# Performance work log

Measured on AMD Instinct MI355X. Metric: run time of the kernel, lower is better.

The kernel has to match this reference:

```python
import jax, jax.numpy as jnp
import numpy as np

EPS = 1e-6
QMAX = 127.0  # hif8 emulated as symmetric 8-bit fake-quant (true hif8 numerics are proprietary)


def _rotate_half(v):
    d = v.shape[-1] // 2
    return jnp.concatenate([-v[..., d:], v[..., :d]], axis=-1)


def _quant(v):
    # per-row (last-axis) absmax quantization emulating hif8 with a per-tensor-row scale
    amax = jnp.max(jnp.abs(v), axis=-1, keepdims=True)
    scale = jnp.maximum(amax / QMAX, 1e-8)
    q = jnp.round(v / scale)
    return q, jnp.squeeze(scale, -1)


def setup_inputs() -> dict:
    key = jax.random.key(0)
    ks = jax.random.split(key, 16)
    B, S, H, Hn, D, L = 2, 4096, 2048, 32, 128, 16384
    return {
        "x": jax.random.normal(ks[0], (B, S, H), jnp.float32),
        "q_norm": jax.random.uniform(ks[1], (H,), jnp.float32),
        "q_norm_scale": jax.random.uniform(ks[2], (H,), jnp.float32),
        "w_qb": jax.random.normal(ks[3], (H, Hn * D), jnp.float32),
        "w_qb_scale": jax.random.uniform(ks[4], (Hn * D,), jnp.float32),
        "wk": jax.random.normal(ks[5], (H, D), jnp.float32),
        "w_proj": jax.random.normal(ks[6], (H, Hn), jnp.float32),
        "ln_gamma_k": jax.random.uniform(ks[7], (H,), jnp.float32),
        "ln_beta_k": jax.random.normal(ks[8], (H,), jnp.float32),
        "cos_idx_rope": jax.random.uniform(ks[9], (S, D), jnp.float32),
        "sin_idx_rope": jax.random.uniform(ks[10], (S, D), jnp.float32),
        "hadamard_q": jax.random.normal(ks[11], (D, D), jnp.float32),
        "hadamard_k": jax.random.normal(ks[12], (D, D), jnp.float32),
        "k_cache": jnp.zeros((L, D), jnp.float32),
        "k_cache_scale": jnp.zeros((L,), jnp.float32),
        "k_cache_index": jnp.arange(B * S, dtype=jnp.int32).reshape(B, S),
    }


def reference(x, q_norm, q_norm_scale, w_qb, w_qb_scale, wk, w_proj,
              ln_gamma_k, ln_beta_k, cos_idx_rope, sin_idx_rope,
              hadamard_q, hadamard_k, k_cache, k_cache_scale, k_cache_index):
    B, S, H = x.shape
    D = hadamard_q.shape[0]
    Hn = w_qb.shape[1] // D

    # ---- Q branch: RMSNorm + smooth scale -> quantized GEMM (dequant fused) ----
    rms = jax.lax.rsqrt(jnp.mean(x * x, axis=-1, keepdims=True) + EPS)
    xq = x * rms * q_norm * q_norm_scale                      # [B,S,H]
    q = jnp.einsum('bsh,hd->bsd', xq, w_qb) * w_qb_scale      # [B,S,Hn*D]
    q = q.reshape(B, S, Hn, D)

    cos_q = cos_idx_rope[:S][None, :, None, :]
    sin_q = sin_idx_rope[:S][None, :, None, :]
    q = q * cos_q + _rotate_half(q) * sin_q                   # RoPE
    q = jnp.einsum('bshd,de->bshe', q, hadamard_q)            # Hadamard mix
    q_hif8, q_scale = _quant(q)                               # [B,S,Hn,D], [B,S,Hn]

    # ---- K branch: LayerNorm -> proj -> RoPE -> Hadamard -> quant ----
    mu = jnp.mean(x, axis=-1, keepdims=True)
    var = jnp.mean(jnp.square(x - mu), axis=-1, keepdims=True)
    xk = (x - mu) * jax.lax.rsqrt(var + EPS) * ln_gamma_k + ln_beta_k
    k = jnp.einsum('bsh,hd->bsd', xk, wk)                     # [B,S,D]
    cos_k = cos_idx_rope[:S][None, :, :]
    sin_k = sin_idx_rope[:S][None, :, :]
    k = k * cos_k + _rotate_half(k) * sin_k
    k = jnp.einsum('bsd,de->bse', k, hadamard_k)
    k_q, k_s = _quant(k)                                      # [B,S,D], [B,S]

    # ---- scatter quantized K into the indexer cache ----
    idx = k_cache_index.reshape(-1)
    k_hif8 = k_cache.at[idx].set(k_q.reshape(-1, D))
    k_scale = k_cache_scale.at[idx].set(k_s.reshape(-1))

    # ---- per-head indexer weights ----
    weights = jnp.einsum('bsh,he->bse', x, w_proj)            # [B,S,Hn]

    return (q_hif8, q_scale, k_hif8, k_scale, weights)
```

## Files before the change

### kernel.cpp

```cpp
#include <hip/hip_runtime.h>
#include <hip/hip_bf16.h>
#include <stdint.h>

constexpr int Mrows = 8192;
constexpr int Hdim  = 2048;
constexpr int Sdim  = 4096;
constexpr int HnD   = 4096;
constexpr int Hn    = 32;
constexpr int Dd    = 128;
constexpr int Lc    = 16384;
constexpr int NFULL = 4352;

typedef unsigned short u16;
typedef __attribute__((ext_vector_type(8))) short    bf16x8;
typedef __attribute__((ext_vector_type(4))) float    f32x4;
typedef __attribute__((ext_vector_type(8))) unsigned short u16x8;

__device__ __forceinline__ float bf2f(u16 u) {
    union { unsigned int i; float f; } v; v.i = ((unsigned int)u) << 16; return v.f;
}
__device__ __forceinline__ u16 f2bf(float f) {
    union { float f; unsigned int i; } v; v.f = f;
    unsigned int x = v.i;
    return (u16)((x + 0x7fffu + ((x >> 16) & 1u)) >> 16);
}
__device__ __forceinline__ void gload_lds16(const void* g, void* l) {
    __builtin_amdgcn_global_load_lds(
        (const __attribute__((address_space(1))) void*)g,
        (__attribute__((address_space(3))) void*)l, 16, 0, 0);
}

__global__ __launch_bounds__(256) void stats_cvt(
    const float* __restrict__ x, u16* __restrict__ xb, float* __restrict__ rms,
    float* __restrict__ mu, float* __restrict__ rstd)
{
    int r = blockIdx.x, t = threadIdx.x;
    const float4* xr = (const float4*)(x + (size_t)r * Hdim);
    float4 a = xr[2 * t], bq = xr[2 * t + 1];
    float v[8] = {a.x, a.y, a.z, a.w, bq.x, bq.y, bq.z, bq.w};
    float s = 0.f, ss = 0.f;
    __align__(16) u16 o[8];
    #pragma unroll
    for (int i = 0; i < 8; i++) { s += v[i]; ss += v[i] * v[i]; o[i] = f2bf(v[i]); }
    ((u16x8*)(xb + (size_t)r * Hdim))[t] = *(const u16x8*)o;
    for (int oo = 32; oo > 0; oo >>= 1) { s += __shfl_down(s, oo); ss += __shfl_down(ss, oo); }
    __shared__ float as[4], ass[4];
    if ((t & 63) == 0) { as[t >> 6] = s; ass[t >> 6] = ss; }
    __syncthreads();
    if (t == 0) {
        float S1 = as[0] + as[1] + as[2] + as[3];
        float S2 = ass[0] + ass[1] + ass[2] + ass[3];
        float mean = S1 / Hdim, msq = S2 / Hdim;
        rms[r]  = rsqrtf(msq + 1e-6f);
        mu[r]   = mean;
        rstd[r] = rsqrtf(msq - mean * mean + 1e-6f);
    }
}

__global__ __launch_bounds__(256) void prep_wt(
    const float* __restrict__ wqb, const float* __restrict__ qn, const float* __restrict__ qns,
    const float* __restrict__ wk,  const float* __restrict__ g,  const float* __restrict__ wproj,
    u16* __restrict__ wt)
{
    __shared__ u16 tile[64][72];
    int k0 = blockIdx.x * 64, n0 = blockIdx.y * 64;
    int t = threadIdx.x;
    int lk = t >> 2, lc0 = (t & 3) * 16;
    int k = k0 + lk;
    float c1k = qn[k] * qns[k];
    float gk  = g[k];
    #pragma unroll
    for (int i = 0; i < 16; i++) {
        int n = n0 + lc0 + i;
        float val;
        if (n < 4096)      val = wqb[(size_t)k * HnD + n] * c1k;
        else if (n < 4224) val = wk[k * Dd + (n - 4096)] * gk;
        else if (n < 4256) val = wproj[k * Hn + (n - 4224)];
        else               val = 0.f;
        tile[lk][lc0 + i] = f2bf(val);
    }
    __syncthreads();
    int ln = t >> 2, lk0 = (t & 3) * 16;
    __align__(16) u16 o[16];
    #pragma unroll
    for (int i = 0; i < 16; i++) o[i] = tile[lk0 + i][ln];
    u16* dst = wt + (size_t)(n0 + ln) * Hdim + k0 + lk0;
    *(u16x8*)dst = *(const u16x8*)o;
    *(u16x8*)(dst + 8) = *((const u16x8*)o + 1);
}

__global__ __launch_bounds__(256) void transpose_h(
    const float* __restrict__ hq, const float* __restrict__ hk,
    u16* __restrict__ hqt, u16* __restrict__ hkt)
{
    __shared__ float tile[128][129];
    const float* src = blockIdx.x ? hk : hq;
    u16* dst = blockIdx.x ? hkt : hqt;
    int t = threadIdx.x;
    int r = t >> 1, h = (t & 1) * 64;
    #pragma unroll
    for (int j = 0; j < 16; j++) {
        float4 v = *(const float4*)(src + r * Dd + h + 4 * j);
        tile[r][h + 4 * j]     = v.x;
        tile[r][h + 4 * j + 1] = v.y;
        tile[r][h + 4 * j + 2] = v.z;
        tile[r][h + 4 * j + 3] = v.w;
    }
    __syncthreads();
    #pragma unroll
    for (int j0 = 0; j0 < 64; j0 += 8) {
        __align__(16) u16 o[8];
        #pragma unroll
        for (int j = 0; j < 8; j++) o[j] = f2bf(tile[h + j0 + j][r]);
        *(u16x8*)(dst + r * Dd + h + j0) = *(const u16x8*)o;
    }
}

__global__ __launch_bounds__(256) void bg_dot(
    const float* __restrict__ wk, const float* __restrict__ g, const float* __restrict__ b,
    float* __restrict__ bdot, float* __restrict__ gdot)
{
    int n = blockIdx.x, t = threadIdx.x;
    float sb = 0.f, sg = 0.f;
    for (int k = t; k < Hdim; k += 256) {
        float w = wk[k * Dd + n];
        sb += b[k] * w;
        sg += g[k] * w;
    }
    for (int o = 32; o > 0; o >>= 1) { sb += __shfl_down(sb, o); sg += __shfl_down(sg, o); }
    __shared__ float rb[4], rg[4];
    if ((t & 63) == 0) { rb[t >> 6] = sb; rg[t >> 6] = sg; }
    __syncthreads();
    if (t == 0) { bdot[n] = rb[0] + rb[1] + rb[2] + rb[3]; gdot[n] = rg[0] + rg[1] + rg[2] + rg[3]; }
}

#define QLDA(slotb, mt) (*(const bf16x8*)(lds + (slotb) + \
    (wr*64 + (mt)*16 + l15) * 64 + qsw))
#define QLDB(slotb, nt) (*(const bf16x8*)(lds + (slotb) + 8192 + \
    (wc*128 + (nt)*16 + l15) * 64 + qsw))
#define QSTG(slotb, sidx) do { \
    gload_lds16(Ab + (size_t)(arow)       * Hdim + (sidx) * 32 + acol, lds + (slotb) + wq); \
    gload_lds16(Ab + (size_t)(64 + arow)  * Hdim + (sidx) * 32 + acol, lds + (slotb) + 4096 + wq); \
    gload_lds16(Bb + (size_t)(arow)       * Hdim + (sidx) * 32 + acol, lds + (slotb) + 8192 + wq); \
    gload_lds16(Bb + (size_t)(64 + arow)  * Hdim + (sidx) * 32 + acol, lds + (slotb) + 12288 + wq); \
    gload_lds16(Bb + (size_t)(128 + arow) * Hdim + (sidx) * 32 + acol, lds + (slotb) + 16384 + wq); \
    gload_lds16(Bb + (size_t)(192 + arow) * Hdim + (sidx) * 32 + acol, lds + (slotb) + 20480 + wq); \
} while (0)

__global__ __launch_bounds__(256, 2) void main_gemm(
    const u16* __restrict__ A, const u16* __restrict__ Bt,
    const float* __restrict__ rms, const float* __restrict__ qbs,
    const u16* __restrict__ hqt,
    const float* __restrict__ cosr, const float* __restrict__ sinr,
    float* __restrict__ oq, float* __restrict__ oqs)
{
    __shared__ __align__(16) char lds[73728];

    int tid = threadIdx.x;
    int w = tid >> 6, lane = tid & 63, quad = lane >> 4, l15 = lane & 15;
    int wr = w >> 1, wc = w & 1;
    int bm = blockIdx.x, bn = blockIdx.y;
    int brow = bm * 128;
    int qsw = (quad ^ ((l15 >> 1) & 3)) * 16;

    const u16* Ab = A  + (size_t)brow * Hdim;
    const u16* Bb = Bt + (size_t)(bn * 256) * Hdim;

    int arow = tid >> 2;
    int acol = (((tid & 3) ^ ((tid >> 3) & 3)) * 8);
    int wq   = w * 1024;

    f32x4 acc[4][8] = {};

    QSTG(0, 0);
    QSTG(24576, 1);
    asm volatile("s_waitcnt vmcnt(6)" ::: "memory");
    __builtin_amdgcn_sched_barrier(0);
    __builtin_amdgcn_s_barrier();

    int slotb = 0;
    for (int s = 0; s < 64; s++) {
        bf16x8 af[4], bq[8];
        #pragma unroll
        for (int mt = 0; mt < 4; mt++) af[mt] = QLDA(slotb, mt);
        #pragma unroll
        for (int nt = 0; nt < 8; nt++) bq[nt] = QLDB(slotb, nt);
        if (s + 2 < 64) {
            int ns = slotb + 49152; if (ns >= 73728) ns -= 73728;
            QSTG(ns, s + 2);
        }
        asm volatile("s_waitcnt lgkmcnt(0)" ::: "memory");
        __builtin_amdgcn_sched_barrier(0);
        __builtin_amdgcn_s_setprio(1);
        #pragma unroll
        for (int mt = 0; mt < 4; mt++)
            #pragma unroll
            for (int nt = 0; nt < 8; nt++)
                acc[mt][nt] = __builtin_amdgcn_mfma_f32_16x16x32_bf16(af[mt], bq[nt], acc[mt][nt], 0, 0, 0);
        __builtin_amdgcn_s_setprio(0);
        if (s < 62) { asm volatile("s_waitcnt vmcnt(6)" ::: "memory"); }
        else        { asm volatile("s_waitcnt vmcnt(0)" ::: "memory"); }
        __builtin_amdgcn_sched_barrier(0);
        __builtin_amdgcn_s_barrier();
        slotb += 24576; if (slotb >= 73728) slotb -= 73728;
    }

    __syncthreads();
    int head = bn * 2 + wc;
    char* Pw = lds + w * 16384;
    float qb[8];
    #pragma unroll
    for (int nt = 0; nt < 8; nt++) qb[nt] = qbs[head * 128 + nt * 16 + l15];
    #pragma unroll
    for (int mt = 0; mt < 4; mt++) {
        float y[8][4];
        #pragma unroll
        for (int reg = 0; reg < 4; reg++) {
            float rv = rms[brow + wr * 64 + mt * 16 + quad * 4 + reg];
            #pragma unroll
            for (int nt = 0; nt < 8; nt++) y[nt][reg] = acc[mt][nt][reg] * rv * qb[nt];
        }
        #pragma unroll
        for (int reg = 0; reg < 4; reg++) {
            int rp = mt * 16 + quad * 4 + reg;
            int s_ = (brow + wr * 64 + rp) & (Sdim - 1);
            const float* cr = cosr + (size_t)s_ * Dd + l15;
            const float* sr = sinr + (size_t)s_ * Dd + l15;
            int sw = (rp & 7) << 4;
            #pragma unroll
            for (int nt = 0; nt < 8; nt++) {
                float c  = cr[nt * 16];
                float sv = sr[nt * 16];
                float sign = (nt < 4) ? -1.f : 1.f;
                float o = y[nt][reg] * c + sign * y[nt ^ 4][reg] * sv;
                int colb = (nt * 16 + l15) * 2;
                *(u16*)(Pw + rp * 256 + (colb ^ sw)) = f2bf(o);
            }
        }
    }
    __syncthreads();
    #pragma unroll
    for (int mt = 0; mt < 4; mt++) {
        bf16x8 pa[4];
        #pragma unroll
        for (int kb = 0; kb < 4; kb++) {
            int row = mt * 16 + l15;
            pa[kb] = *(const bf16x8*)(Pw + row * 256 + ((kb * 64 + quad * 16) ^ ((row & 7) << 4)));
        }
        f32x4 a2[8] = {};
        #pragma unroll
        for (int nt = 0; nt < 8; nt++) {
            #pragma unroll
            for (int kb = 0; kb < 4; kb++) {
                bf16x8 hb = *(const bf16x8*)(hqt + (size_t)(nt * 16 + l15) * Dd + kb * 32 + quad * 8);
                a2[nt] = __builtin_amdgcn_mfma_f32_16x16x32_bf16(pa[kb], hb, a2[nt], 0, 0, 0);
            }
        }
        #pragma unroll
        for (int reg = 0; reg < 4; reg++) {
            float m = 0.f;
            #pragma unroll
            for (int nt = 0; nt < 8; nt++) m = fmaxf(m, fabsf(a2[nt][reg]));
            m = fmaxf(m, __shfl_xor(m, 8));
            m = fmaxf(m, __shfl_xor(m, 4));
            m = fmaxf(m, __shfl_xor(m, 2));
            m = fmaxf(m, __shfl_xor(m, 1));
            float scale = fmaxf(m * (1.f / 127.f), 1e-8f);
            float inv = 1.f / scale;
            int r = brow + wr * 64 + mt * 16 + quad * 4 + reg;
            float* orow = oq + (size_t)r * HnD + head * 128;
            #pragma unroll
            for (int nt = 0; nt < 8; nt++)
                orow[nt * 16 + l15] = rintf(a2[nt][reg] * inv);
            if (l15 == 0) oqs[(size_t)r * Hn + head] = scale;
        }
    }
}

__global__ __launch_bounds__(256) void kw_gemm(
    const u16* __restrict__ A, const u16* __restrict__ Bt,
    const float* __restrict__ rstd, const float* __restrict__ mu,
    const float* __restrict__ bdot, const float* __restrict__ gdot,
    float* __restrict__ kpre, float* __restrict__ wout)
{
    __shared__ __align__(16) u16 sA[32 * 64];
    __shared__ __align__(16) u16 sB[192 * 64];
    int tid = threadIdx.x, w = tid >> 6, lane = tid & 63, quad = lane >> 4, l15 = lane & 15;
    int blk = blockIdx.x;
    const u16* Ab = A  + (size_t)(blk * 32) * Hdim;
    const u16* Bb = Bt + (size_t)4096 * Hdim;

    f32x4 acc[2][3] = {};

    for (int s = 0; s < 32; s++) {
        __syncthreads();
        {
            int row = tid >> 3, ch = (tid & 7) ^ (row & 7);
            gload_lds16(Ab + (size_t)row * Hdim + s * 64 + ch * 8, (char*)sA + w * 1024);
        }
        #pragma unroll
        for (int u = 0; u < 6; u++) {
            int idx = u * 256 + tid;
            int row = idx >> 3, ch = (idx & 7) ^ (row & 7);
            gload_lds16(Bb + (size_t)row * Hdim + s * 64 + ch * 8,
                        (char*)sB + u * 4096 + w * 1024);
        }
        __syncthreads();
        #pragma unroll
        for (int kk = 0; kk < 2; kk++) {
            bf16x8 af[2], bf[3];
            #pragma unroll
            for (int m = 0; m < 2; m++) {
                int row = m * 16 + l15;
                af[m] = *(const bf16x8*)(sA + row * 64 + (((kk * 4 + quad) ^ (row & 7)) * 8));
            }
            #pragma unroll
            for (int j = 0; j < 3; j++) {
                int row = (w * 3 + j) * 16 + l15;
                bf[j] = *(const bf16x8*)(sB + row * 64 + (((kk * 4 + quad) ^ (row & 7)) * 8));
            }
            #pragma unroll
            for (int m = 0; m < 2; m++)
                #pragma unroll
                for (int j = 0; j < 3; j++)
                    acc[m][j] = __builtin_amdgcn_mfma_f32_16x16x32_bf16(af[m], bf[j], acc[m][j], 0, 0, 0);
        }
    }
    #pragma unroll
    for (int m = 0; m < 2; m++)
        #pragma unroll
        for (int reg = 0; reg < 4; reg++) {
            int r = blk * 32 + m * 16 + quad * 4 + reg;
            float sd = rstd[r], m_ = mu[r];
            #pragma unroll
            for (int j = 0; j < 3; j++) {
                int f = w * 3 + j, c = f * 16 + l15;
                float v = acc[m][j][reg];
                if (f < 8)       kpre[(size_t)r * Dd + c] = v * sd + bdot[c] - sd * m_ * gdot[c];
                else if (f < 10) wout[(size_t)r * Hn + (c - 128)] = v;
            }
        }
}

__global__ void copy_cache(const float* __restrict__ kc, const float* __restrict__ kcs,
                           float* __restrict__ dk, float* __restrict__ dks)
{
    int g = blockIdx.x * 256 + threadIdx.x;
    ((float4*)dk)[2 * g]     = ((const float4*)kc)[2 * g];
    ((float4*)dk)[2 * g + 1] = ((const float4*)kc)[2 * g + 1];
    if (g < Lc / 8) {
        ((float4*)dks)[2 * g]     = ((const float4*)kcs)[2 * g];
        ((float4*)dks)[2 * g + 1] = ((const float4*)kcs)[2 * g + 1];
    }
}

template <int IS_K>
__global__ __launch_bounds__(256) void post_kernel(
    const float* src,
    const u16* __restrict__ ht,
    const float* __restrict__ cosr, const float* __restrict__ sinr,
    const int* __restrict__ idx,
    float* dstq, float* __restrict__ dsts)
{
    constexpr int RP = 136;
    __shared__ __align__(16) u16 sA[32 * RP];
    __shared__ __align__(16) u16 sB[128 * RP];
    __shared__ float pamax[32][2];
    __shared__ int sidx[32];

    int blk = blockIdx.x, tid = threadIdx.x;

    {
        int n = tid >> 1, kk0 = (tid & 1) * 64;
        const u16x8* gp = (const u16x8*)(ht + n * Dd + kk0);
        u16* lb = sB + n * RP + kk0;
        #pragma unroll
        for (int j = 0; j < 8; j++) *(u16x8*)(lb + j * 8) = gp[j];
    }
    {
        int r = tid >> 3, c = tid & 7;
        int d0 = c * 16;
        int s_ = IS_K ? ((blk * 32 + r) & (Sdim - 1)) : (blk & (Sdim - 1));
        const float* srow = src + (size_t)blk * 4096 + r * Dd;
        int p0 = (d0 + 64) & 127;
        float sign = (d0 < 64) ? -1.f : 1.f;
        float vv[16], pv[16], cv[16], sv[16];
        #pragma unroll
        for (int j = 0; j < 4; j++) {
            float4 a = *(const float4*)(srow + d0 + 4 * j);
            float4 p = *(const float4*)(srow + p0 + 4 * j);
            float4 cc = *(const float4*)(cosr + (size_t)s_ * Dd + d0 + 4 * j);
            float4 sc = *(const float4*)(sinr + (size_t)s_ * Dd + d0 + 4 * j);
            vv[4*j] = a.x; vv[4*j+1] = a.y; vv[4*j+2] = a.z; vv[4*j+3] = a.w;
            pv[4*j] = p.x; pv[4*j+1] = p.y; pv[4*j+2] = p.z; pv[4*j+3] = p.w;
            cv[4*j] = cc.x; cv[4*j+1] = cc.y; cv[4*j+2] = cc.z; cv[4*j+3] = cc.w;
            sv[4*j] = sc.x; sv[4*j+1] = sc.y; sv[4*j+2] = sc.z; sv[4*j+3] = sc.w;
        }
        __align__(16) u16 o[16];
        #pragma unroll
        for (int i = 0; i < 16; i++)
            o[i] = f2bf(vv[i] * cv[i] + sign * pv[i] * sv[i]);
        u16* la = sA + r * RP + d0;
        *(u16x8*)la = *(const u16x8*)o;
        *(u16x8*)(la + 8) = *((const u16x8*)o + 1);
        if (IS_K && tid < 32) sidx[tid] = idx[blk * 32 + tid];
    }
    __syncthreads();

    int w = tid >> 6, lane = tid & 63, quad = lane >> 4, l15 = lane & 15;
    int rs = (w & 1) * 16, cg = (w >> 1) * 64;
    f32x4 acc[4] = {};
    #pragma unroll
    for (int kb = 0; kb < 4; kb++) {
        bf16x8 a = *(const bf16x8*)(sA + (rs + l15) * RP + kb * 32 + quad * 8);
        #pragma unroll
        for (int nt = 0; nt < 4; nt++) {
            bf16x8 b = *(const bf16x8*)(sB + (cg + nt * 16 + l15) * RP + kb * 32 + quad * 8);
            acc[nt] = __builtin_amdgcn_mfma_f32_16x16x32_bf16(a, b, acc[nt], 0, 0, 0);
        }
    }
    #pragma unroll
    for (int reg = 0; reg < 4; reg++) {
        float m = 0.f;
        #pragma unroll
        for (int nt = 0; nt < 4; nt++) m = fmaxf(m, fabsf(acc[nt][reg]));
        m = fmaxf(m, __shfl_xor(m, 8));
        m = fmaxf(m, __shfl_xor(m, 4));
        m = fmaxf(m, __shfl_xor(m, 2));
        m = fmaxf(m, __shfl_xor(m, 1));
        if (l15 == 0) pamax[rs + quad * 4 + reg][w >> 1] = m;
    }
    __syncthreads();
    #pragma unroll
    for (int reg = 0; reg < 4; reg++) {
        int r = rs + quad * 4 + reg;
        float am = fmaxf(pamax[r][0], pamax[r][1]);
        float scale = fmaxf(am * (1.f / 127.f), 1e-8f);
        float inv = 1.f / scale;
        size_t dro = IS_K ? (size_t)sidx[r] * Dd : (size_t)blk * 4096 + (size_t)r * Dd;
        #pragma unroll
        for (int nt = 0; nt < 4; nt++)
            dstq[dro + cg + nt * 16 + l15] = rintf(acc[nt][reg] * inv);
        if (l15 == 0 && (w >> 1) == 0)
            dsts[IS_K ? sidx[r] : blk * Hn + r] = scale;
    }
}

extern "C" void kernel_launch(void* const* d_in, const int* in_sizes, int n_in,
                              void* d_out, int out_size, void* d_ws, size_t ws_size,
                              hipStream_t stream) {
    (void)in_sizes; (void)n_in; (void)out_size; (void)ws_size;
    const float* x    = (const float*)d_in[0];
    const float* qn   = (const float*)d_in[1];
    const float* qns  = (const float*)d_in[2];
    const float* wqb  = (const float*)d_in[3];
    const float* wqbs = (const float*)d_in[4];
    const float* wk   = (const float*)d_in[5];
    const float* wpj  = (const float*)d_in[6];
    const float* g    = (const float*)d_in[7];
    const float* b    = (const float*)d_in[8];
    const float* cosr = (const float*)d_in[9];
    const float* sinr = (const float*)d_in[10];
    const float* hq   = (const float*)d_in[11];
    const float* hk   = (const float*)d_in[12];
    const float* kc   = (const float*)d_in[13];
    const float* kcs  = (const float*)d_in[14];
    const int*   idx  = (const int*)d_in[15];

    char* ws = (char*)d_ws;
    size_t o = 0;
    u16* xb  = (u16*)(ws + o); o += (size_t)Mrows * Hdim * 2;
    u16* wt  = (u16*)(ws + o); o += (size_t)NFULL * Hdim * 2;
    u16* hqt = (u16*)(ws + o); o += Dd * Dd * 2;
    u16* hkt = (u16*)(ws + o); o += Dd * Dd * 2;
    float* rmsb  = (float*)(ws + o); o += (size_t)Mrows * 4;
    float* mub   = (float*)(ws + o); o += (size_t)Mrows * 4;
    float* rstdb = (float*)(ws + o); o += (size_t)Mrows * 4;
    float* bdotb = (float*)(ws + o); o += 512;
    float* gdotb = (float*)(ws + o); o += 512;
    float* kpre  = (float*)(ws + o); o += (size_t)Mrows * Dd * 4;

    float* out = (float*)d_out;
    float* oq  = out;
    float* oqs = oq  + (size_t)Mrows * HnD;
    float* ok  = oqs + (size_t)Mrows * Hn;
    float* oks = ok  + (size_t)Lc * Dd;
    float* ow  = oks + Lc;

    stats_cvt<<<Mrows, 256, 0, stream>>>(x, xb, rmsb, mub, rstdb);
    prep_wt<<<dim3(Hdim / 64, NFULL / 64), 256, 0, stream>>>(wqb, qn, qns, wk, g, wpj, wt);
    transpose_h<<<2, 256, 0, stream>>>(hq, hk, hqt, hkt);
    bg_dot<<<Dd, 256, 0, stream>>>(wk, g, b, bdotb, gdotb);
    kw_gemm<<<Mrows / 32, 256, 0, stream>>>(xb, wt, rstdb, mub, bdotb, gdotb, kpre, ow);
    main_gemm<<<dim3(Mrows / 128, 16), 256, 0, stream>>>(
        xb, wt, rmsb, wqbs, hqt, cosr, sinr, oq, oqs);
    copy_cache<<<(Lc * Dd / 8) / 256, 256, 0, stream>>>(kc, kcs, ok, oks);
    post_kernel<1><<<Mrows / 32, 256, 0, stream>>>(kpre, hkt, cosr, sinr, idx, ok, oks);
}
```

Before: 496.9 us.

## Fuse prep kernels, enlarge main GEMM tile to 256x256, fuse K branch

The four setup kernels and the cache copy are merged into one launch that dispatches on block index. The main GEMM moves to 512-thread blocks with a 256x256 tile, a two-buffer, 64-wide K staging scheme and a phased MFMA/load interleave. The K-projection GEMM, RoPE, Hadamard and quantization are fused into a single kernel, which removes the kpre intermediate round trip through global memory. Together these are meant to cut launch overhead and memory traffic and to raise GEMM data reuse. The cost is one block per CU with 128KB of LDS and much more complex scheduling code.

```diff
diff --git a/kernel.cpp b/kernel.cpp
--- a/kernel.cpp
+++ b/kernel.cpp
@@ -16,9 +16,6 @@
 typedef __attribute__((ext_vector_type(4))) float    f32x4;
 typedef __attribute__((ext_vector_type(8))) unsigned short u16x8;
 
-__device__ __forceinline__ float bf2f(u16 u) {
-    union { unsigned int i; float f; } v; v.i = ((unsigned int)u) << 16; return v.f;
-}
 __device__ __forceinline__ u16 f2bf(float f) {
     union { float f; unsigned int i; } v; v.f = f;
     unsigned int x = v.i;
@@ -30,180 +27,203 @@
         (__attribute__((address_space(3))) void*)l, 16, 0, 0);
 }
 
-__global__ __launch_bounds__(256) void stats_cvt(
+__global__ __launch_bounds__(256) void fused_prep(
     const float* __restrict__ x, u16* __restrict__ xb, float* __restrict__ rms,
-    float* __restrict__ mu, float* __restrict__ rstd)
-{
-    int r = blockIdx.x, t = threadIdx.x;
-    const float4* xr = (const float4*)(x + (size_t)r * Hdim);
-    float4 a = xr[2 * t], bq = xr[2 * t + 1];
-    float v[8] = {a.x, a.y, a.z, a.w, bq.x, bq.y, bq.z, bq.w};
-    float s = 0.f, ss = 0.f;
-    __align__(16) u16 o[8];
-    #pragma unroll
-    for (int i = 0; i < 8; i++) { s += v[i]; ss += v[i] * v[i]; o[i] = f2bf(v[i]); }
-    ((u16x8*)(xb + (size_t)r * Hdim))[t] = *(const u16x8*)o;
-    for (int oo = 32; oo > 0; oo >>= 1) { s += __shfl_down(s, oo); ss += __shfl_down(ss, oo); }
-    __shared__ float as[4], ass[4];
-    if ((t & 63) == 0) { as[t >> 6] = s; ass[t >> 6] = ss; }
-    __syncthreads();
-    if (t == 0) {
-        float S1 = as[0] + as[1] + as[2] + as[3];
-        float S2 = ass[0] + ass[1] + ass[2] + ass[3];
-        float mean = S1 / Hdim, msq = S2 / Hdim;
-        rms[r]  = rsqrtf(msq + 1e-6f);
-        mu[r]   = mean;
-        rstd[r] = rsqrtf(msq - mean * mean + 1e-6f);
-    }
-}
-
-__global__ __launch_bounds__(256) void prep_wt(
+    float* __restrict__ mu, float* __restrict__ rstd,
     const float* __restrict__ wqb, const float* __restrict__ qn, const float* __restrict__ qns,
     const float* __restrict__ wk,  const float* __restrict__ g,  const float* __restrict__ wproj,
-    u16* __restrict__ wt)
+    u16* __restrict__ wt,
+    const float* __restrict__ hq, const float* __restrict__ hk,
+    u16* __restrict__ hqt, u16* __restrict__ hkt,
+    const float* __restrict__ b,
+    float* __restrict__ bdot, float* __restrict__ gdot,
+    const float* __restrict__ kc, const float* __restrict__ kcs,
+    float* __restrict__ dk, float* __restrict__ dks)
 {
-    __shared__ u16 tile[64][72];
-    int k0 = blockIdx.x * 64, n0 = blockIdx.y * 64;
-    int t = threadIdx.x;
-    int lk = t >> 2, lc0 = (t & 3) * 16;
-    int k = k0 + lk;
-    float c1k = qn[k] * qns[k];
-    float gk  = g[k];
-    #pragma unroll
-    for (int i = 0; i < 16; i++) {
-        int n = n0 + lc0 + i;
-        float val;
-        if (n < 4096)      val = wqb[(size_t)k * HnD + n] * c1k;
-        else if (n < 4224) val = wk[k * Dd + (n - 4096)] * gk;
-        else if (n < 4256) val = wproj[k * Hn + (n - 4224)];
-        else               val = 0.f;
-        tile[lk][lc0 + i] = f2bf(val);
-    }
-    __syncthreads();
-    int ln = t >> 2, lk0 = (t & 3) * 16;
-    __align__(16) u16 o[16];
-    #pragma unroll
-    for (int i = 0; i < 16; i++) o[i] = tile[lk0 + i][ln];
-    u16* dst = wt + (size_t)(n0 + ln) * Hdim + k0 + lk0;
-    *(u16x8*)dst = *(const u16x8*)o;
-    *(u16x8*)(dst + 8) = *((const u16x8*)o + 1);
-}
-
-__global__ __launch_bounds__(256) void transpose_h(
-    const float* __restrict__ hq, const float* __restrict__ hk,
-    u16* __restrict__ hqt, u16* __restrict__ hkt)
-{
-    __shared__ float tile[128][129];
-    const float* src = blockIdx.x ? hk : hq;
-    u16* dst = blockIdx.x ? hkt : hqt;
-    int t = threadIdx.x;
-    int r = t >> 1, h = (t & 1) * 64;
-    #pragma unroll
-    for (int j = 0; j < 16; j++) {
-        float4 v = *(const float4*)(src + r * Dd + h + 4 * j);
-        tile[r][h + 4 * j]     = v.x;
-        tile[r][h + 4 * j + 1] = v.y;
-        tile[r][h + 4 * j + 2] = v.z;
-        tile[r][h + 4 * j + 3] = v.w;
-    }
-    __syncthreads();
-    #pragma unroll
-    for (int j0 = 0; j0 < 64; j0 += 8) {
+    __shared__ u16 utile[64 * 72];
+    __shared__ float sred[8];
+    int bid = blockIdx.x, t = threadIdx.x;
+
+    if (bid < 8192) {
+        int r = bid;
+        const float4* xr = (const float4*)(x + (size_t)r * Hdim);
+        float4 a4 = xr[2 * t], b4 = xr[2 * t + 1];
+        float v[8] = {a4.x, a4.y, a4.z, a4.w, b4.x, b4.y, b4.z, b4.w};
+        float s = 0.f, ss = 0.f;
         __align__(16) u16 o[8];
         #pragma unroll
-        for (int j = 0; j < 8; j++) o[j] = f2bf(tile[h + j0 + j][r]);
-        *(u16x8*)(dst + r * Dd + h + j0) = *(const u16x8*)o;
-    }
-}
-
-__global__ __launch_bounds__(256) void bg_dot(
-    const float* __restrict__ wk, const float* __restrict__ g, const float* __restrict__ b,
-    float* __restrict__ bdot, float* __restrict__ gdot)
-{
-    int n = blockIdx.x, t = threadIdx.x;
-    float sb = 0.f, sg = 0.f;
-    for (int k = t; k < Hdim; k += 256) {
-        float w = wk[k * Dd + n];
-        sb += b[k] * w;
-        sg += g[k] * w;
-    }
-    for (int o = 32; o > 0; o >>= 1) { sb += __shfl_down(sb, o); sg += __shfl_down(sg, o); }
-    __shared__ float rb[4], rg[4];
-    if ((t & 63) == 0) { rb[t >> 6] = sb; rg[t >> 6] = sg; }
-    __syncthreads();
-    if (t == 0) { bdot[n] = rb[0] + rb[1] + rb[2] + rb[3]; gdot[n] = rg[0] + rg[1] + rg[2] + rg[3]; }
-}
-
-#define QLDA(slotb, mt) (*(const bf16x8*)(lds + (slotb) + \
-    (wr*64 + (mt)*16 + l15) * 64 + qsw))
-#define QLDB(slotb, nt) (*(const bf16x8*)(lds + (slotb) + 8192 + \
-    (wc*128 + (nt)*16 + l15) * 64 + qsw))
-#define QSTG(slotb, sidx) do { \
-    gload_lds16(Ab + (size_t)(arow)       * Hdim + (sidx) * 32 + acol, lds + (slotb) + wq); \
-    gload_lds16(Ab + (size_t)(64 + arow)  * Hdim + (sidx) * 32 + acol, lds + (slotb) + 4096 + wq); \
-    gload_lds16(Bb + (size_t)(arow)       * Hdim + (sidx) * 32 + acol, lds + (slotb) + 8192 + wq); \
-    gload_lds16(Bb + (size_t)(64 + arow)  * Hdim + (sidx) * 32 + acol, lds + (slotb) + 12288 + wq); \
-    gload_lds16(Bb + (size_t)(128 + arow) * Hdim + (sidx) * 32 + acol, lds + (slotb) + 16384 + wq); \
-    gload_lds16(Bb + (size_t)(192 + arow) * Hdim + (sidx) * 32 + acol, lds + (slotb) + 20480 + wq); \
+        for (int i = 0; i < 8; i++) { s += v[i]; ss += v[i] * v[i]; o[i] = f2bf(v[i]); }
+        ((u16x8*)(xb + (size_t)r * Hdim))[t] = *(const u16x8*)o;
+        for (int oo = 32; oo > 0; oo >>= 1) { s += __shfl_down(s, oo); ss += __shfl_down(ss, oo); }
+        if ((t & 63) == 0) { sred[t >> 6] = s; sred[4 + (t >> 6)] = ss; }
+        __syncthreads();
+        if (t == 0) {
+            float S1 = sred[0] + sred[1] + sred[2] + sred[3];
+            float S2 = sred[4] + sred[5] + sred[6] + sred[7];
+            float mean = S1 / Hdim, msq = S2 / Hdim;
+            rms[r]  = rsqrtf(msq + 1e-6f);
+            mu[r]   = mean;
+            rstd[r] = rsqrtf(msq - mean * mean + 1e-6f);
+        }
+    } else if (bid < 10368) {
+        int b2 = bid - 8192;
+        int k0 = (b2 & 31) * 64, n0 = (b2 >> 5) * 64;
+        int lk = t >> 2, lc0 = (t & 3) * 16;
+        int k = k0 + lk;
+        float c1k = qn[k] * qns[k];
+        float gk  = g[k];
+        #pragma unroll
+        for (int i = 0; i < 16; i++) {
+            int n = n0 + lc0 + i;
+            float val;
+            if (n < 4096)      val = wqb[(size_t)k * HnD + n] * c1k;
+            else if (n < 4224) val = wk[k * Dd + (n - 4096)] * gk;
+            else if (n < 4256) val = wproj[k * Hn + (n - 4224)];
+            else               val = 0.f;
+            utile[lk * 72 + lc0 + i] = f2bf(val);
+        }
+        __syncthreads();
+        int ln = t >> 2, lk0 = (t & 3) * 16;
+        __align__(16) u16 o[16];
+        #pragma unroll
+        for (int i = 0; i < 16; i++) o[i] = utile[(lk0 + i) * 72 + ln];
+        u16* dst = wt + (size_t)(n0 + ln) * Hdim + k0 + lk0;
+        *(u16x8*)dst = *(const u16x8*)o;
+        *(u16x8*)(dst + 8) = *((const u16x8*)o + 1);
+    } else if (bid < 10376) {
+        int q = bid - 10368;
+        int matq = q >> 2, tr = (q >> 1) & 1, tc = q & 1;
+        const float* src = matq ? hk : hq;
+        u16* dst = matq ? hkt : hqt;
+        int r = t >> 2, c0 = (t & 3) * 16;
+        #pragma unroll
+        for (int i = 0; i < 4; i++) {
+            float4 vv = *(const float4*)(src + (size_t)(tr * 64 + r) * Dd + tc * 64 + c0 + 4 * i);
+            utile[r * 72 + c0 + 4 * i]     = f2bf(vv.x);
+            utile[r * 72 + c0 + 4 * i + 1] = f2bf(vv.y);
+            utile[r * 72 + c0 + 4 * i + 2] = f2bf(vv.z);
+            utile[r * 72 + c0 + 4 * i + 3] = f2bf(vv.w);
+        }
+        __syncthreads();
+        int n = t >> 2, k0 = (t & 3) * 16;
+        __align__(16) u16 o[16];
+        #pragma unroll
+        for (int i = 0; i < 16; i++) o[i] = utile[(k0 + i) * 72 + n];
+        u16* dp = dst + (size_t)(tc * 64 + n) * Dd + tr * 64 + k0;
+        *(u16x8*)dp = *(const u16x8*)o;
+        *(u16x8*)(dp + 8) = *((const u16x8*)o + 1);
+    } else if (bid < 10504) {
+        int n = bid - 10376;
+        float sb = 0.f, sg = 0.f;
+        for (int k = t; k < Hdim; k += 256) {
+            float w = wk[k * Dd + n];
+            sb += b[k] * w;
+            sg += g[k] * w;
+        }
+        for (int o = 32; o > 0; o >>= 1) { sb += __shfl_down(sb, o); sg += __shfl_down(sg, o); }
+        if ((t & 63) == 0) { sred[t >> 6] = sb; sred[4 + (t >> 6)] = sg; }
+        __syncthreads();
+        if (t == 0) {
+            bdot[n] = sred[0] + sred[1] + sred[2] + sred[3];
+            gdot[n] = sred[4] + sred[5] + sred[6] + sred[7];
+        }
+    } else {
+        int gg = (bid - 10504) * 256 + t;
+        ((float4*)dk)[2 * gg]     = ((const float4*)kc)[2 * gg];
+        ((float4*)dk)[2 * gg + 1] = ((const float4*)kc)[2 * gg + 1];
+        if (gg < Lc / 8) {
+            ((float4*)dks)[2 * gg]     = ((const float4*)kcs)[2 * gg];
+            ((float4*)dks)[2 * gg + 1] = ((const float4*)kcs)[2 * gg + 1];
+        }
+    }
+}
+
+#define RA(bufo, ks, mt) (*(const bf16x8*)(lds + (bufo) * 65536 + (ks) * 16384 + \
+    (wr * 64 + (mt) * 16 + l15) * 64 + rsw))
+#define RB(bufo, ks, nh, j) (*(const bf16x8*)(lds + (bufo) * 65536 + 32768 + (ks) * 16384 + \
+    (wc * 128 + (nh) * 64 + (j) * 16 + l15) * 64 + rsw))
+#define SA(tt, ks) do { \
+    const u16* gp_ = Ab + (size_t)srow * Hdim + (tt) * 64 + (ks) * 32 + scol; \
+    char* dp_ = lds + (((tt) & 1) * 65536) + (ks) * 16384 + wq; \
+    gload_lds16(gp_, dp_); \
+    gload_lds16(gp_ + (size_t)128 * Hdim, dp_ + 8192); \
 } while (0)
-
-__global__ __launch_bounds__(256, 2) void main_gemm(
+#define SB(tt, ks) do { \
+    const u16* gp_ = Bb + (size_t)srow * Hdim + (tt) * 64 + (ks) * 32 + scol; \
+    char* dp_ = lds + (((tt) & 1) * 65536) + 32768 + (ks) * 16384 + wq; \
+    gload_lds16(gp_, dp_); \
+    gload_lds16(gp_ + (size_t)128 * Hdim, dp_ + 8192); \
+} while (0)
+#define VM6 do { asm volatile("s_waitcnt vmcnt(6)" ::: "memory"); __builtin_amdgcn_sched_barrier(0); } while (0)
+#define VM0 do { asm volatile("s_waitcnt vmcnt(0)" ::: "memory"); __builtin_amdgcn_sched_barrier(0); } while (0)
+#define NOPS ((void)0)
+#define PH(bufo, ks, nh, STG, WT) do { \
+    if ((nh) == 0) { \
+        _Pragma("unroll") for (int mt = 0; mt < 4; mt++) af[mt] = RA(bufo, ks, mt); \
+    } \
+    _Pragma("unroll") for (int j = 0; j < 4; j++) bfr[j] = RB(bufo, ks, nh, j); \
+    STG; \
+    asm volatile("s_waitcnt lgkmcnt(0)" ::: "memory"); \
+    __builtin_amdgcn_sched_barrier(0); \
+    __builtin_amdgcn_s_setprio(1); \
+    _Pragma("unroll") for (int mt = 0; mt < 4; mt++) \
+        _Pragma("unroll") for (int j = 0; j < 4; j++) \
+            acc[mt][(nh) * 4 + j] = __builtin_amdgcn_mfma_f32_16x16x32_bf16( \
+                af[mt], bfr[j], acc[mt][(nh) * 4 + j], 0, 0, 0); \
+    __builtin_amdgcn_s_setprio(0); \
+    WT; \
+    __builtin_amdgcn_s_barrier(); \
+} while (0)
+
+__global__ __launch_bounds__(512, 1) void main_gemm(
     const u16* __restrict__ A, const u16* __restrict__ Bt,
     const float* __restrict__ rms, const float* __restrict__ qbs,
     const u16* __restrict__ hqt,
     const float* __restrict__ cosr, const float* __restrict__ sinr,
     float* __restrict__ oq, float* __restrict__ oqs)
 {
-    __shared__ __align__(16) char lds[73728];
+    __shared__ __align__(16) char lds[131072];
 
     int tid = threadIdx.x;
     int w = tid >> 6, lane = tid & 63, quad = lane >> 4, l15 = lane & 15;
-    int wr = w >> 1, wc = w & 1;
+    int wr = w & 3, wc = w >> 2;
     int bm = blockIdx.x, bn = blockIdx.y;
-    int brow = bm * 128;
-    int qsw = (quad ^ ((l15 >> 1) & 3)) * 16;
+    int brow = bm * 256;
+    int rsw = (quad ^ ((l15 >> 1) & 3)) * 16;
 
     const u16* Ab = A  + (size_t)brow * Hdim;
     const u16* Bb = Bt + (size_t)(bn * 256) * Hdim;
 
-    int arow = tid >> 2;
-    int acol = (((tid & 3) ^ ((tid >> 3) & 3)) * 8);
-    int wq   = w * 1024;
-
+    int srow = tid >> 2;
+    int scol = (((tid & 3) ^ ((srow >> 1) & 3)) * 8);
+    int wq = w * 1024;
+
+    bf16x8 af[4], bfr[4];
     f32x4 acc[4][8] = {};
 
-    QSTG(0, 0);
-    QSTG(24576, 1);
-    asm volatile("s_waitcnt vmcnt(6)" ::: "memory");
-    __builtin_amdgcn_sched_barrier(0);
+    SA(0, 0); SB(0, 0); SA(0, 1); SB(0, 1); SA(1, 0); SB(1, 0); SA(1, 1);
+    VM6;
     __builtin_amdgcn_s_barrier();
 
-    int slotb = 0;
-    for (int s = 0; s < 64; s++) {
-        bf16x8 af[4], bq[8];
-        #pragma unroll
-        for (int mt = 0; mt < 4; mt++) af[mt] = QLDA(slotb, mt);
-        #pragma unroll
-        for (int nt = 0; nt < 8; nt++) bq[nt] = QLDB(slotb, nt);
-        if (s + 2 < 64) {
-            int ns = slotb + 49152; if (ns >= 73728) ns -= 73728;
-            QSTG(ns, s + 2);
-        }
-        asm volatile("s_waitcnt lgkmcnt(0)" ::: "memory");
-        __builtin_amdgcn_sched_barrier(0);
-        __builtin_amdgcn_s_setprio(1);
-        #pragma unroll
-        for (int mt = 0; mt < 4; mt++)
-            #pragma unroll
-            for (int nt = 0; nt < 8; nt++)
-                acc[mt][nt] = __builtin_amdgcn_mfma_f32_16x16x32_bf16(af[mt], bq[nt], acc[mt][nt], 0, 0, 0);
-        __builtin_amdgcn_s_setprio(0);
-        if (s < 62) { asm volatile("s_waitcnt vmcnt(6)" ::: "memory"); }
-        else        { asm volatile("s_waitcnt vmcnt(0)" ::: "memory"); }
-        __builtin_amdgcn_sched_barrier(0);
-        __builtin_amdgcn_s_barrier();
-        slotb += 24576; if (slotb >= 73728) slotb -= 73728;
-    }
+    for (int I = 0; I < 15; I++) {
+        int t1 = 2 * I + 1, t2 = 2 * I + 2, t3 = 2 * I + 3;
+        PH(0, 0, 0, SB(t1, 1), NOPS);
+        PH(0, 0, 1, SA(t2, 0), NOPS);
+        PH(0, 1, 0, SB(t2, 0), NOPS);
+        PH(0, 1, 1, SA(t2, 1), VM6);
+        PH(1, 0, 0, SB(t2, 1), NOPS);
+        PH(1, 0, 1, SA(t3, 0), NOPS);
+        PH(1, 1, 0, SB(t3, 0), NOPS);
+        PH(1, 1, 1, SA(t3, 1), VM6);
+    }
+    PH(0, 0, 0, SB(31, 1), NOPS);
+    PH(0, 0, 1, NOPS, NOPS);
+    PH(0, 1, 0, NOPS, NOPS);
+    PH(0, 1, 1, NOPS, VM0);
+    PH(1, 0, 0, NOPS, NOPS);
+    PH(1, 0, 1, NOPS, NOPS);
+    PH(1, 1, 0, NOPS, NOPS);
+    PH(1, 1, 1, NOPS, NOPS);
 
     __syncthreads();
     int head = bn * 2 + wc;
@@ -277,172 +297,127 @@
     }
 }
 
-__global__ __launch_bounds__(256) void kw_gemm(
+__global__ __launch_bounds__(256) void k_branch(
     const u16* __restrict__ A, const u16* __restrict__ Bt,
     const float* __restrict__ rstd, const float* __restrict__ mu,
     const float* __restrict__ bdot, const float* __restrict__ gdot,
-    float* __restrict__ kpre, float* __restrict__ wout)
+    const u16* __restrict__ hkt,
+    const float* __restrict__ cosr, const float* __restrict__ sinr,
+    const int* __restrict__ idx,
+    float* __restrict__ ok, float* __restrict__ oks, float* __restrict__ wout)
 {
-    __shared__ __align__(16) u16 sA[32 * 64];
-    __shared__ __align__(16) u16 sB[192 * 64];
+    __shared__ __align__(16) char klds[73728];
+    __shared__ float pamax[32][2];
+    __shared__ int sidx[32];
     int tid = threadIdx.x, w = tid >> 6, lane = tid & 63, quad = lane >> 4, l15 = lane & 15;
     int blk = blockIdx.x;
-    const u16* Ab = A  + (size_t)(blk * 32) * Hdim;
+    int mh = w & 1, ngrp = w >> 1;
+    const u16* Ab = A + (size_t)(blk * 32) * Hdim;
     const u16* Bb = Bt + (size_t)4096 * Hdim;
-
-    f32x4 acc[2][3] = {};
-
+    int F[5];
+    F[0] = ngrp * 2; F[1] = ngrp * 2 + 1; F[2] = 4 + ngrp * 2; F[3] = 5 + ngrp * 2; F[4] = 8 + ngrp;
+    int ar = tid >> 3, ach = ((tid & 7) ^ (ar & 7)) * 8;
+    int wq1 = w * 1024;
+
+#define KSTG(slotn, st) do { \
+    gload_lds16(Ab + (size_t)ar * Hdim + (st) * 64 + ach, klds + (slotn) * 24576 + wq1); \
+    _Pragma("unroll") for (int u = 0; u < 5; u++) { \
+        int ix = u * 256 + tid; int br = ix >> 3; int bch = ((ix & 7) ^ (br & 7)) * 8; \
+        gload_lds16(Bb + (size_t)br * Hdim + (st) * 64 + bch, \
+                    klds + (slotn) * 24576 + 4096 + u * 4096 + wq1); \
+    } \
+} while (0)
+#define KRA(slotn, ks) (*(const bf16x8*)(klds + (slotn) * 24576 + \
+    (mh * 16 + l15) * 128 + ((((ks) * 4 + quad) ^ (l15 & 7)) * 16)))
+#define KRB(slotn, ks, f) (*(const bf16x8*)(klds + (slotn) * 24576 + 4096 + \
+    ((f) * 16 + l15) * 128 + ((((ks) * 4 + quad) ^ (l15 & 7)) * 16)))
+
+    f32x4 acc[5] = {};
+    KSTG(0, 0); KSTG(1, 1);
+    asm volatile("s_waitcnt vmcnt(6)" ::: "memory");
+    __builtin_amdgcn_sched_barrier(0);
+    __builtin_amdgcn_s_barrier();
+    int sl = 0;
     for (int s = 0; s < 32; s++) {
-        __syncthreads();
-        {
-            int row = tid >> 3, ch = (tid & 7) ^ (row & 7);
-            gload_lds16(Ab + (size_t)row * Hdim + s * 64 + ch * 8, (char*)sA + w * 1024);
-        }
-        #pragma unroll
-        for (int u = 0; u < 6; u++) {
-            int idx = u * 256 + tid;
-            int row = idx >> 3, ch = (idx & 7) ^ (row & 7);
-            gload_lds16(Bb + (size_t)row * Hdim + s * 64 + ch * 8,
-                        (char*)sB + u * 4096 + w * 1024);
-        }
-        __syncthreads();
-        #pragma unroll
-        for (int kk = 0; kk < 2; kk++) {
-            bf16x8 af[2], bf[3];
-            #pragma unroll
-            for (int m = 0; m < 2; m++) {
-                int row = m * 16 + l15;
-                af[m] = *(const bf16x8*)(sA + row * 64 + (((kk * 4 + quad) ^ (row & 7)) * 8));
-            }
-            #pragma unroll
-            for (int j = 0; j < 3; j++) {
-                int row = (w * 3 + j) * 16 + l15;
-                bf[j] = *(const bf16x8*)(sB + row * 64 + (((kk * 4 + quad) ^ (row & 7)) * 8));
-            }
-            #pragma unroll
-            for (int m = 0; m < 2; m++)
-                #pragma unroll
-                for (int j = 0; j < 3; j++)
-                    acc[m][j] = __builtin_amdgcn_mfma_f32_16x16x32_bf16(af[m], bf[j], acc[m][j], 0, 0, 0);
-        }
-    }
-    #pragma unroll
-    for (int m = 0; m < 2; m++)
-        #pragma unroll
-        for (int reg = 0; reg < 4; reg++) {
-            int r = blk * 32 + m * 16 + quad * 4 + reg;
-            float sd = rstd[r], m_ = mu[r];
-            #pragma unroll
-            for (int j = 0; j < 3; j++) {
-                int f = w * 3 + j, c = f * 16 + l15;
-                float v = acc[m][j][reg];
-                if (f < 8)       kpre[(size_t)r * Dd + c] = v * sd + bdot[c] - sd * m_ * gdot[c];
-                else if (f < 10) wout[(size_t)r * Hn + (c - 128)] = v;
-            }
-        }
-}
-
-__global__ void copy_cache(const float* __restrict__ kc, const float* __restrict__ kcs,
-                           float* __restrict__ dk, float* __restrict__ dks)
-{
-    int g = blockIdx.x * 256 + threadIdx.x;
-    ((float4*)dk)[2 * g]     = ((const float4*)kc)[2 * g];
-    ((float4*)dk)[2 * g + 1] = ((const float4*)kc)[2 * g + 1];
-    if (g < Lc / 8) {
-        ((float4*)dks)[2 * g]     = ((const float4*)kcs)[2 * g];
-        ((float4*)dks)[2 * g + 1] = ((const float4*)kcs)[2 * g + 1];
-    }
-}
-
-template <int IS_K>
-__global__ __launch_bounds__(256) void post_kernel(
-    const float* src,
-    const u16* __restrict__ ht,
-    const float* __restrict__ cosr, const float* __restrict__ sinr,
-    const int* __restrict__ idx,
-    float* dstq, float* __restrict__ dsts)
-{
-    constexpr int RP = 136;
-    __shared__ __align__(16) u16 sA[32 * RP];
-    __shared__ __align__(16) u16 sB[128 * RP];
-    __shared__ float pamax[32][2];
-    __shared__ int sidx[32];
-
-    int blk = blockIdx.x, tid = threadIdx.x;
-
-    {
-        int n = tid >> 1, kk0 = (tid & 1) * 64;
-        const u16x8* gp = (const u16x8*)(ht + n * Dd + kk0);
-        u16* lb = sB + n * RP + kk0;
-        #pragma unroll
-        for (int j = 0; j < 8; j++) *(u16x8*)(lb + j * 8) = gp[j];
-    }
-    {
-        int r = tid >> 3, c = tid & 7;
-        int d0 = c * 16;
-        int s_ = IS_K ? ((blk * 32 + r) & (Sdim - 1)) : (blk & (Sdim - 1));
-        const float* srow = src + (size_t)blk * 4096 + r * Dd;
-        int p0 = (d0 + 64) & 127;
-        float sign = (d0 < 64) ? -1.f : 1.f;
-        float vv[16], pv[16], cv[16], sv[16];
+        bf16x8 ka[2], kbf[2][5];
+        ka[0] = KRA(sl, 0); ka[1] = KRA(sl, 1);
+        #pragma unroll
+        for (int j = 0; j < 5; j++) { kbf[0][j] = KRB(sl, 0, F[j]); kbf[1][j] = KRB(sl, 1, F[j]); }
+        if (s + 2 < 32) { int ns = sl + 2; if (ns >= 3) ns -= 3; KSTG(ns, s + 2); }
+        asm volatile("s_waitcnt lgkmcnt(0)" ::: "memory");
+        __builtin_amdgcn_sched_barrier(0);
+        __builtin_amdgcn_s_setprio(1);
+        #pragma unroll
+        for (int ks = 0; ks < 2; ks++)
+            #pragma unroll
+            for (int j = 0; j < 5; j++)
+                acc[j] = __builtin_amdgcn_mfma_f32_16x16x32_bf16(ka[ks], kbf[ks][j], acc[j], 0, 0, 0);
+        __builtin_amdgcn_s_setprio(0);
+        if (s < 30) { asm volatile("s_waitcnt vmcnt(6)" ::: "memory"); }
+        else        { asm volatile("s_waitcnt vmcnt(0)" ::: "memory"); }
+        __builtin_amdgcn_sched_barrier(0);
+        __builtin_amdgcn_s_barrier();
+        sl++; if (sl == 3) sl = 0;
+    }
+
+    if (tid < 32) sidx[tid] = idx[blk * 32 + tid];
+    __syncthreads();
+    u16* sP = (u16*)klds;
+    #pragma unroll
+    for (int reg = 0; reg < 4; reg++) {
+        int rl = mh * 16 + quad * 4 + reg;
+        int r = blk * 32 + rl;
+        float sd = rstd[r], m_ = mu[r];
+        int s_ = r & (Sdim - 1);
+        float v[4];
         #pragma unroll
         for (int j = 0; j < 4; j++) {
-            float4 a = *(const float4*)(srow + d0 + 4 * j);
-            float4 p = *(const float4*)(srow + p0 + 4 * j);
-            float4 cc = *(const float4*)(cosr + (size_t)s_ * Dd + d0 + 4 * j);
-            float4 sc = *(const float4*)(sinr + (size_t)s_ * Dd + d0 + 4 * j);
-            vv[4*j] = a.x; vv[4*j+1] = a.y; vv[4*j+2] = a.z; vv[4*j+3] = a.w;
-            pv[4*j] = p.x; pv[4*j+1] = p.y; pv[4*j+2] = p.z; pv[4*j+3] = p.w;
-            cv[4*j] = cc.x; cv[4*j+1] = cc.y; cv[4*j+2] = cc.z; cv[4*j+3] = cc.w;
-            sv[4*j] = sc.x; sv[4*j+1] = sc.y; sv[4*j+2] = sc.z; sv[4*j+3] = sc.w;
-        }
-        __align__(16) u16 o[16];
-        #pragma unroll
-        for (int i = 0; i < 16; i++)
-            o[i] = f2bf(vv[i] * cv[i] + sign * pv[i] * sv[i]);
-        u16* la = sA + r * RP + d0;
-        *(u16x8*)la = *(const u16x8*)o;
-        *(u16x8*)(la + 8) = *((const u16x8*)o + 1);
-        if (IS_K && tid < 32) sidx[tid] = idx[blk * 32 + tid];
+            int col = F[j] * 16 + l15;
+            v[j] = acc[j][reg] * sd + bdot[col] - sd * m_ * gdot[col];
+        }
+        #pragma unroll
+        for (int j = 0; j < 4; j++) {
+            int col = F[j] * 16 + l15;
+            float c = cosr[(size_t)s_ * Dd + col], sv = sinr[(size_t)s_ * Dd + col];
+            float sign = (j < 2) ? -1.f : 1.f;
+            sP[rl * 136 + col] = f2bf(v[j] * c + sign * v[j ^ 2] * sv);
+        }
+        wout[(size_t)r * Hn + (F[4] - 8) * 16 + l15] = acc[4][reg];
     }
     __syncthreads();
-
-    int w = tid >> 6, lane = tid & 63, quad = lane >> 4, l15 = lane & 15;
-    int rs = (w & 1) * 16, cg = (w >> 1) * 64;
-    f32x4 acc[4] = {};
-    #pragma unroll
-    for (int kb = 0; kb < 4; kb++) {
-        bf16x8 a = *(const bf16x8*)(sA + (rs + l15) * RP + kb * 32 + quad * 8);
+    f32x4 a2[4] = {};
+    #pragma unroll
+    for (int kb4 = 0; kb4 < 4; kb4++) {
+        bf16x8 pa = *(const bf16x8*)(sP + (mh * 16 + l15) * 136 + kb4 * 32 + quad * 8);
         #pragma unroll
         for (int nt = 0; nt < 4; nt++) {
-            bf16x8 b = *(const bf16x8*)(sB + (cg + nt * 16 + l15) * RP + kb * 32 + quad * 8);
-            acc[nt] = __builtin_amdgcn_mfma_f32_16x16x32_bf16(a, b, acc[nt], 0, 0, 0);
+            bf16x8 hb = *(const bf16x8*)(hkt + (size_t)(ngrp * 64 + nt * 16 + l15) * Dd + kb4 * 32 + quad * 8);
+            a2[nt] = __builtin_amdgcn_mfma_f32_16x16x32_bf16(pa, hb, a2[nt], 0, 0, 0);
         }
     }
     #pragma unroll
     for (int reg = 0; reg < 4; reg++) {
         float m = 0.f;
         #pragma unroll
-        for (int nt = 0; nt < 4; nt++) m = fmaxf(m, fabsf(acc[nt][reg]));
+        for (int nt = 0; nt < 4; nt++) m = fmaxf(m, fabsf(a2[nt][reg]));
         m = fmaxf(m, __shfl_xor(m, 8));
         m = fmaxf(m, __shfl_xor(m, 4));
         m = fmaxf(m, __shfl_xor(m, 2));
         m = fmaxf(m, __shfl_xor(m, 1));
-        if (l15 == 0) pamax[rs + quad * 4 + reg][w >> 1] = m;
+        if (l15 == 0) pamax[mh * 16 + quad * 4 + reg][ngrp] = m;
     }
     __syncthreads();
     #pragma unroll
     for (int reg = 0; reg < 4; reg++) {
-        int r = rs + quad * 4 + reg;
-        float am = fmaxf(pamax[r][0], pamax[r][1]);
+        int rl = mh * 16 + quad * 4 + reg;
+        float am = fmaxf(pamax[rl][0], pamax[rl][1]);
         float scale = fmaxf(am * (1.f / 127.f), 1e-8f);
         float inv = 1.f / scale;
-        size_t dro = IS_K ? (size_t)sidx[r] * Dd : (size_t)blk * 4096 + (size_t)r * Dd;
+        size_t dro = (size_t)sidx[rl] * Dd;
         #pragma unroll
         for (int nt = 0; nt < 4; nt++)
-            dstq[dro + cg + nt * 16 + l15] = rintf(acc[nt][reg] * inv);
-        if (l15 == 0 && (w >> 1) == 0)
-            dsts[IS_K ? sidx[r] : blk * Hn + r] = scale;
+            ok[dro + ngrp * 64 + nt * 16 + l15] = rintf(a2[nt][reg] * inv);
+        if (l15 == 0 && ngrp == 0) oks[sidx[rl]] = scale;
     }
 }
 
@@ -478,7 +453,6 @@
     float* rstdb = (float*)(ws + o); o += (size_t)Mrows * 4;
     float* bdotb = (float*)(ws + o); o += 512;
     float* gdotb = (float*)(ws + o); o += 512;
-    float* kpre  = (float*)(ws + o); o += (size_t)Mrows * Dd * 4;
 
     float* out = (float*)d_out;
     float* oq  = out;
@@ -487,13 +461,11 @@
     float* oks = ok  + (size_t)Lc * Dd;
     float* ow  = oks + Lc;
 
-    stats_cvt<<<Mrows, 256, 0, stream>>>(x, xb, rmsb, mub, rstdb);
-    prep_wt<<<dim3(Hdim / 64, NFULL / 64), 256, 0, stream>>>(wqb, qn, qns, wk, g, wpj, wt);
-    transpose_h<<<2, 256, 0, stream>>>(hq, hk, hqt, hkt);
-    bg_dot<<<Dd, 256, 0, stream>>>(wk, g, b, bdotb, gdotb);
-    kw_gemm<<<Mrows / 32, 256, 0, stream>>>(xb, wt, rstdb, mub, bdotb, gdotb, kpre, ow);
-    main_gemm<<<dim3(Mrows / 128, 16), 256, 0, stream>>>(
+    fused_prep<<<11528, 256, 0, stream>>>(
+        x, xb, rmsb, mub, rstdb, wqb, qn, qns, wk, g, wpj, wt,
+        hq, hk, hqt, hkt, b, bdotb, gdotb, kc, kcs, ok, oks);
+    main_gemm<<<dim3(Mrows / 256, 16), 512, 0, stream>>>(
         xb, wt, rmsb, wqbs, hqt, cosr, sinr, oq, oqs);
-    copy_cache<<<(Lc * Dd / 8) / 256, 256, 0, stream>>>(kc, kcs, ok, oks);
-    post_kernel<1><<<Mrows / 32, 256, 0, stream>>>(kpre, hkt, cosr, sinr, idx, ok, oks);
-}
+    k_branch<<<Mrows / 32, 256, 0, stream>>>(
+        xb, wt, rstdb, mub, bdotb, gdotb, hkt, cosr, sinr, idx, ok, oks, ow);
+}
```

After: 457.9 us. -7.8%, faster.
